# Optimization experiments

Measured on AMD Instinct MI355X. Metric: run time of the kernel, lower is better.

Reference implementation:

```python
import jax, jax.numpy as jnp
import numpy as np

DIM = 256
D_STATE = 32
EXPAND = 2
E = EXPAND * DIM            # d_inner = 512
DT_RANK = (DIM + 15) // 16  # 16 (mamba default ceil(d_model/16))
D_CONV = 4                  # mamba default causal conv width
B = 4
L = 1024


def layernorm(x, g, b, eps=1e-5):
    m = jnp.mean(x, axis=-1, keepdims=True)
    v = jnp.var(x, axis=-1, keepdims=True)
    return (x - m) / jnp.sqrt(v + eps) * g + b


def dwconv(x_bcl, w, b, pad):
    # x_bcl: [B,C,L], w: [C,1,K] depthwise
    y = jax.lax.conv_general_dilated(
        x_bcl, w, window_strides=(1,), padding=[pad],
        feature_group_count=x_bcl.shape[1],
        dimension_numbers=('NCW', 'OIW', 'NCW'))
    return y + b[None, :, None]


def selective_scan(u, dt, A, Bm, Cm, D):
    # u,dt: [B,L,E]; A: [E,N]; Bm,Cm: [B,L,N]; D: [E]
    dA = jnp.exp(dt[..., None] * A)                                # [B,L,E,N]
    dBu = dt[..., None] * Bm[:, :, None, :] * u[..., None]         # [B,L,E,N]

    def step(h, inp):
        dA_t, dBu_t = inp
        h = dA_t * h + dBu_t
        return h, h

    h0 = jnp.zeros((u.shape[0], E, D_STATE), u.dtype)
    _, hs = jax.lax.scan(step, h0, (dA.transpose(1, 0, 2, 3), dBu.transpose(1, 0, 2, 3)))
    y = jnp.einsum('lben,bln->ble', hs, Cm)                        # [B,L,E]
    return y + u * D


def mamba(x, in_proj_w, ssm_conv_w, ssm_conv_b, x_proj_w,
          dt_proj_w, dt_proj_b, A_log, Dp, out_proj_w):
    xz = x @ in_proj_w.T                     # [B,L,2E]
    xin, z = xz[..., :E], xz[..., E:]
    # causal depthwise conv (pad left D_CONV-1) + SiLU
    xc = dwconv(xin.transpose(0, 2, 1), ssm_conv_w, ssm_conv_b, (D_CONV - 1, 0))
    u = jax.nn.silu(xc).transpose(0, 2, 1)   # [B,L,E]
    dbl = u @ x_proj_w.T                      # [B,L,dt_rank+2N]
    dt_r = dbl[..., :DT_RANK]
    Bm = dbl[..., DT_RANK:DT_RANK + D_STATE]
    Cm = dbl[..., DT_RANK + D_STATE:]
    dt = jax.nn.softplus(dt_r @ dt_proj_w.T + dt_proj_b)  # [B,L,E]
    A = -jnp.exp(A_log)                                    # [E,N]
    y = selective_scan(u, dt, A, Bm, Cm, Dp)
    y = y * jax.nn.silu(z)
    return y @ out_proj_w.T


def setup_inputs() -> dict:
    key = jax.random.key(0)
    ks = jax.random.split(key, 12)
    f = lambda k, s, sc=0.02: jax.random.normal(k, s, jnp.float32) * sc
    dt_init = jnp.exp(jax.random.uniform(ks[10], (E,), jnp.float32,
                                         np.log(1e-3), np.log(1e-1)))
    dt_bias = dt_init + jnp.log(-jnp.expm1(-dt_init))  # inverse softplus
    A_log = jnp.log(jnp.tile(jnp.arange(1, D_STATE + 1, dtype=jnp.float32), (E, 1)))
    return {
        'x': jax.random.normal(ks[0], (B, L, DIM), jnp.float32),
        'norm1_g': jnp.ones((DIM,), jnp.float32), 'norm1_b': jnp.zeros((DIM,), jnp.float32),
        'conv_w': f(ks[1], (DIM, 1, 3), 0.1), 'conv_b': jnp.zeros((DIM,), jnp.float32),
        'in_proj_w': f(ks[2], (2 * E, DIM)),
        'ssm_conv_w': f(ks[3], (E, 1, D_CONV), 0.1), 'ssm_conv_b': jnp.zeros((E,), jnp.float32),
        'x_proj_w': f(ks[4], (DT_RANK + 2 * D_STATE, E)),
        'dt_proj_w': f(ks[5], (E, DT_RANK), 0.1), 'dt_proj_b': dt_bias,
        'A_log': A_log, 'Dp': jnp.ones((E,), jnp.float32),
        'out_proj_w': f(ks[6], (DIM, E)),
        'norm2_g': jnp.ones((DIM,), jnp.float32), 'norm2_b': jnp.zeros((DIM,), jnp.float32),
        'mlp_w1': f(ks[7], (4 * DIM, DIM)), 'mlp_b1': jnp.zeros((4 * DIM,), jnp.float32),
        'mlp_w2': f(ks[8], (DIM, 4 * DIM)), 'mlp_b2': jnp.zeros((DIM,), jnp.float32),
    }


def reference(x, norm1_g, norm1_b, conv_w, conv_b, in_proj_w, ssm_conv_w,
              ssm_conv_b, x_proj_w, dt_proj_w, dt_proj_b, A_log, Dp,
              out_proj_w, norm2_g, norm2_b, mlp_w1, mlp_b1, mlp_w2, mlp_b2):
    res = x
    h = layernorm(x, norm1_g, norm1_b)
    # local depthwise conv, kernel 3, same padding
    h_conv = dwconv(h.transpose(0, 2, 1), conv_w, conv_b, (1, 1)).transpose(0, 2, 1)
    h = mamba(h_conv + h, in_proj_w, ssm_conv_w, ssm_conv_b, x_proj_w,
              dt_proj_w, dt_proj_b, A_log, Dp, out_proj_w)
    h = res + h  # drop_path = identity (eval)
    m = layernorm(h, norm2_g, norm2_b)
    m = jax.nn.gelu(m @ mlp_w1.T + mlp_b1, approximate=False) @ mlp_w2.T + mlp_b2
    return h + m
```

## Files before the change

kernel.cpp:

```cpp
#include <hip/hip_runtime.h>
#include <hip/hip_bf16.h>
#include <math.h>

#define BATCH 4
#define LSEQ  1024
#define DIM   256
#define ESZ   512
#define NST   32
#define RNK   16
#define MROWS 4096
#define NCH   64
#define CHL   16

typedef __attribute__((ext_vector_type(8))) short bf16x8;
typedef __attribute__((ext_vector_type(4))) float f32x4;

__device__ __forceinline__ float silu_f(float v) { return v / (1.f + __expf(-v)); }
__device__ __forceinline__ float softplus_f(float v) {
    return (v > 20.f) ? v : log1pf(__expf(v));
}
__device__ __forceinline__ float bs2f(short s) {
    union { unsigned int u; float f; } v;
    v.u = ((unsigned int)(unsigned short)s) << 16;
    return v.f;
}
__device__ __forceinline__ short f2bs(float f) {
    __hip_bfloat16 h = __float2bfloat16(f);
    return *(short*)&h;
}

__global__ __launch_bounds__(256) void prep_kernel(
    const float* __restrict__ ipw, const float* __restrict__ opw,
    const float* __restrict__ w1,  const float* __restrict__ w2,
    const float* __restrict__ xpw, __hip_bfloat16* __restrict__ dst,
    const float* __restrict__ x, const float* __restrict__ g,
    const float* __restrict__ b, const float* __restrict__ cw,
    const float* __restrict__ cb, __hip_bfloat16* __restrict__ hm)
{
    if (blockIdx.x < 936) {
        int i = blockIdx.x * 256 + threadIdx.x;
        if (i >= 239616) return;
        const float* s; int off;
        if      (i < 65536)  { s = ipw; off = i; }
        else if (i < 98304)  { s = opw; off = i - 65536; }
        else if (i < 163840) { s = w1;  off = i - 98304; }
        else if (i < 229376) { s = w2;  off = i - 163840; }
        else                 { s = xpw; off = i - 229376; }
        float4 v = ((const float4*)s)[off];
        union { __hip_bfloat16 h[4]; short4 s4; } u;
        u.h[0] = __float2bfloat16(v.x);
        u.h[1] = __float2bfloat16(v.y);
        u.h[2] = __float2bfloat16(v.z);
        u.h[3] = __float2bfloat16(v.w);
        ((short4*)dst)[i] = u.s4;
        return;
    }
    const int row = blockIdx.x - 936;
    const int l   = row & (LSEQ - 1);
    const int d   = threadIdx.x;
    const float gc = g[d], bc = b[d];

    float xc = x[row * DIM + d];
    float xl = (l > 0)        ? x[(row - 1) * DIM + d] : 0.f;
    float xr = (l < LSEQ - 1) ? x[(row + 1) * DIM + d] : 0.f;

    float a[6] = { xc, xc * xc, xl, xl * xl, xr, xr * xr };
    #pragma unroll
    for (int o = 32; o > 0; o >>= 1)
        #pragma unroll
        for (int j = 0; j < 6; ++j) a[j] += __shfl_down(a[j], o, 64);
    __shared__ float red[4][6];
    if ((d & 63) == 0)
        #pragma unroll
        for (int j = 0; j < 6; ++j) red[d >> 6][j] = a[j];
    __syncthreads();
    float t[6];
    #pragma unroll
    for (int j = 0; j < 6; ++j)
        t[j] = red[0][j] + red[1][j] + red[2][j] + red[3][j];

    auto ln = [&](float v, float s, float s2) {
        float m  = s * (1.f / DIM);
        float vr = s2 * (1.f / DIM) - m * m;
        return (v - m) * rsqrtf(vr + 1e-5f) * gc + bc;
    };
    float ln_c = ln(xc, t[0], t[1]);
    float acc  = cw[d * 3 + 1] * ln_c + cb[d] + ln_c;
    if (l > 0)        acc += cw[d * 3 + 0] * ln(xl, t[2], t[3]);
    if (l < LSEQ - 1) acc += cw[d * 3 + 2] * ln(xr, t[4], t[5]);
    hm[row * DIM + d] = __float2bfloat16(acc);
}

#define EPI_NONE      0
#define EPI_GELU      2
#define EPI_RES       3
#define EPI_BIAS_RES  4

template <int BM, int BN, int EPI, int OUT_BF16>
__global__ __launch_bounds__(256) void gemm_lds(
    const __hip_bfloat16* __restrict__ A, int lda,
    const __hip_bfloat16* __restrict__ W, int ldw,
    void* __restrict__ Cout, int ldc, int K,
    const float* __restrict__ bias,
    const float* __restrict__ res, int ldres)
{
    constexpr int BK  = 64;
    constexpr int WTN = BN / 4;
    constexpr int BNF = WTN / 16;
    constexpr int AMF = BM / 16;
    constexpr int AIT = (BM * 8) / 256;
    constexpr int WIT = (BN * 8) / 256;

    __shared__ __hip_bfloat16 As[2][BM * BK];
    __shared__ __hip_bfloat16 Ws[2][BN * BK];

    const int tid  = threadIdx.x;
    const int lane = tid & 63;
    const int wave = tid >> 6;
    const int wn   = wave * WTN;
    const int m0   = blockIdx.x * BM;
    const int n0   = blockIdx.y * BN;
    const int q    = lane >> 4;
    const int lr   = lane & 15;
    const int sx   = (lr & 7) << 4;

    const __hip_bfloat16* Ab = A + (long)m0 * lda;
    const __hip_bfloat16* Wb = W + (long)n0 * ldw;

    f32x4 acc[AMF][BNF];
    #pragma unroll
    for (int i = 0; i < AMF; ++i)
        #pragma unroll
        for (int j = 0; j < BNF; ++j)
            acc[i][j] = (f32x4){0.f, 0.f, 0.f, 0.f};

    auto stage = [&](int s, int k0) {
        #pragma unroll
        for (int it = 0; it < AIT; ++it) {
            const int g   = it * 256 + tid;
            const int row = g >> 3;
            const int scc = (g & 7) ^ (row & 7);
            __builtin_amdgcn_global_load_lds(
                (const __attribute__((address_space(1))) void*)
                    (Ab + (long)row * lda + k0 + scc * 8),
                (__attribute__((address_space(3))) void*)
                    (&As[s][(it * 256 + wave * 64) * 8]),
                16, 0, 0);
        }
        #pragma unroll
        for (int it = 0; it < WIT; ++it) {
            const int g   = it * 256 + tid;
            const int row = g >> 3;
            const int scc = (g & 7) ^ (row & 7);
            __builtin_amdgcn_global_load_lds(
                (const __attribute__((address_space(1))) void*)
                    (Wb + (long)row * ldw + k0 + scc * 8),
                (__attribute__((address_space(3))) void*)
                    (&Ws[s][(it * 256 + wave * 64) * 8]),
                16, 0, 0);
        }
    };

    stage(0, 0);
    __syncthreads();

    int cur = 0;
    for (int k0 = 0; k0 < K; k0 += BK) {
        if (k0 + BK < K) stage(cur ^ 1, k0 + BK);
        #pragma unroll
        for (int ks = 0; ks < 2; ++ks) {
            const int co = (ks * 64 + q * 16) ^ sx;
            bf16x8 af[AMF], bfr[BNF];
            #pragma unroll
            for (int i = 0; i < AMF; ++i)
                af[i] = *(const bf16x8*)(
                    (const char*)&As[cur][0] + (i * 16 + lr) * 128 + co);
            #pragma unroll
            for (int j = 0; j < BNF; ++j)
                bfr[j] = *(const bf16x8*)(
                    (const char*)&Ws[cur][0] + (wn + j * 16 + lr) * 128 + co);
            #pragma unroll
            for (int i = 0; i < AMF; ++i)
                #pragma unroll
                for (int j = 0; j < BNF; ++j)
                    acc[i][j] = __builtin_amdgcn_mfma_f32_16x16x32_bf16(
                        af[i], bfr[j], acc[i][j], 0, 0, 0);
        }
        __syncthreads();
        cur ^= 1;
    }

    #pragma unroll
    for (int i = 0; i < AMF; ++i) {
        #pragma unroll
        for (int j = 0; j < BNF; ++j) {
            const int col  = n0 + wn + j * 16 + lr;
            const int rowb = m0 + i * 16 + q * 4;
            #pragma unroll
            for (int r = 0; r < 4; ++r) {
                const int row = rowb + r;
                float v = acc[i][j][r];
                if (EPI == EPI_GELU) {
                    v += bias[col];
                    v = 0.5f * v * (1.f + erff(v * 0.70710678118654752f));
                } else if (EPI == EPI_RES) {
                    v += res[(long)row * ldres + col];
                } else if (EPI == EPI_BIAS_RES) {
                    v += bias[col] + res[(long)row * ldres + col];
                }
                if (OUT_BF16)
                    ((__hip_bfloat16*)Cout)[(long)row * ldc + col] = __float2bfloat16(v);
                else
                    ((float*)Cout)[(long)row * ldc + col] = v;
            }
        }
    }
}

__global__ __launch_bounds__(256) void outproj_ln_kernel(
    const __hip_bfloat16* __restrict__ A,
    const __hip_bfloat16* __restrict__ W,
    const float* __restrict__ xres,
    const float* __restrict__ g, const float* __restrict__ b,
    float* __restrict__ hres,
    __hip_bfloat16* __restrict__ h1)
{
    constexpr int BM = 16, BN = 256, BK = 64, K = 512;
    __shared__ __hip_bfloat16 As[2][BM * BK];
    __shared__ __hip_bfloat16 Ws[2][BN * BK];
    __shared__ float lnt[BM][BN + 4];
    __shared__ float lnm[BM], lni[BM];

    const int tid  = threadIdx.x;
    const int lane = tid & 63;
    const int wave = tid >> 6;
    const int wn   = wave * 64;
    const int m0   = blockIdx.x * BM;
    const int q    = lane >> 4;
    const int lr   = lane & 15;
    const int sx   = (lr & 7) << 4;

    const __hip_bfloat16* Ab = A + (long)m0 * K;

    f32x4 acc[4];
    #pragma unroll
    for (int j = 0; j < 4; ++j) acc[j] = (f32x4){0.f, 0.f, 0.f, 0.f};

    auto stage = [&](int s, int k0) {
        if (wave < 2) {
            const int gA  = tid;
            const int row = gA >> 3;
            const int scc = (gA & 7) ^ (row & 7);
            __builtin_amdgcn_global_load_lds(
                (const __attribute__((address_space(1))) void*)
                    (Ab + (long)row * K + k0 + scc * 8),
                (__attribute__((address_space(3))) void*)
                    (&As[s][(wave * 64) * 8]),
                16, 0, 0);
        }
        #pragma unroll
        for (int it = 0; it < 8; ++it) {
            const int gW  = it * 256 + tid;
            const int row = gW >> 3;
            const int scc = (gW & 7) ^ (row & 7);
            __builtin_amdgcn_global_load_lds(
                (const __attribute__((address_space(1))) void*)
                    (W + (long)row * K + k0 + scc * 8),
                (__attribute__((address_space(3))) void*)
                    (&Ws[s][(it * 256 + wave * 64) * 8]),
                16, 0, 0);
        }
    };

    stage(0, 0);
    __syncthreads();

    int cur = 0;
    for (int k0 = 0; k0 < K; k0 += BK) {
        if (k0 + BK < K) stage(cur ^ 1, k0 + BK);
        #pragma unroll
        for (int ks = 0; ks < 2; ++ks) {
            const int co = (ks * 64 + q * 16) ^ sx;
            bf16x8 af = *(const bf16x8*)((const char*)&As[cur][0] + lr * 128 + co);
            #pragma unroll
            for (int j = 0; j < 4; ++j) {
                bf16x8 bfr = *(const bf16x8*)(
                    (const char*)&Ws[cur][0] + (wn + j * 16 + lr) * 128 + co);
                acc[j] = __builtin_amdgcn_mfma_f32_16x16x32_bf16(af, bfr, acc[j], 0, 0, 0);
            }
        }
        __syncthreads();
        cur ^= 1;
    }

    #pragma unroll
    for (int j = 0; j < 4; ++j) {
        const int col = wn + j * 16 + lr;
        #pragma unroll
        for (int r = 0; r < 4; ++r) {
            const int row = q * 4 + r;
            float v = acc[j][r] + xres[(long)(m0 + row) * DIM + col];
            hres[(long)(m0 + row) * DIM + col] = v;
            lnt[row][col] = v;
        }
    }
    __syncthreads();

    {
        const int rr = tid >> 4, cc = tid & 15;
        float s = 0.f, s2 = 0.f;
        #pragma unroll
        for (int k = 0; k < 16; ++k) {
            float v = lnt[rr][cc + k * 16];
            s += v; s2 += v * v;
        }
        #pragma unroll
        for (int m = 8; m > 0; m >>= 1) {
            s  += __shfl_xor(s,  m, 64);
            s2 += __shfl_xor(s2, m, 64);
        }
        if (cc == 0) {
            float mean = s * (1.f / DIM);
            float var  = s2 * (1.f / DIM) - mean * mean;
            lnm[rr] = mean;
            lni[rr] = rsqrtf(var + 1e-5f);
        }
    }
    __syncthreads();

    #pragma unroll
    for (int j = 0; j < 4; ++j) {
        const int col = wn + j * 16 + lr;
        const float gc = g[col], bc = b[col];
        #pragma unroll
        for (int r = 0; r < 4; ++r) {
            const int row = q * 4 + r;
            float v = lnt[row][col];
            h1[(long)(m0 + row) * DIM + col] =
                __float2bfloat16((v - lnm[row]) * lni[row] * gc + bc);
        }
    }
}

__global__ __launch_bounds__(256) void xproj_conv_mfma(
    const __hip_bfloat16* __restrict__ xz,
    const float* __restrict__ scw, const float* __restrict__ scb,
    const __hip_bfloat16* __restrict__ W,
    float* __restrict__ C)
{
    constexpr int LS = 72;
    __shared__ __hip_bfloat16 As[64 * LS];
    __shared__ __hip_bfloat16 Ws[80 * LS];
    const int tid  = threadIdx.x;
    const int lane = tid & 63;
    const int wave = tid >> 6;
    const int wm   = wave * 16;
    const int m0   = blockIdx.x * 64;
    const int srow = tid >> 3;
    const int scol = (tid & 7) * 8;
    const int q    = lane >> 4;
    const int lr   = lane & 15;

    f32x4 acc[5];
    #pragma unroll
    for (int j = 0; j < 5; ++j) acc[j] = (f32x4){0.f, 0.f, 0.f, 0.f};

    auto mk_u2 = [&](int k0, bf16x8& u0, bf16x8& u1) {
        const int e0 = k0 + scol;
        float4 w4[8]; float cbv[8];
        #pragma unroll
        for (int j = 0; j < 8; ++j) {
            w4[j]  = *(const float4*)(scw + (e0 + j) * 4);
            cbv[j] = scb[e0 + j];
        }
        #pragma unroll
        for (int r = 0; r < 2; ++r) {
            const int bl = m0 + r * 32 + srow;
            const int l  = bl & (LSEQ - 1);
            const __hip_bfloat16* xp = xz + (long)bl * 1024 + e0;
            bf16x8 x3 = *(const bf16x8*)(xp);
            bf16x8 x0 = (l >= 3) ? *(const bf16x8*)(xp - 3 * 1024) : (bf16x8){0,0,0,0,0,0,0,0};
            bf16x8 x1 = (l >= 2) ? *(const bf16x8*)(xp - 2 * 1024) : (bf16x8){0,0,0,0,0,0,0,0};
            bf16x8 x2 = (l >= 1) ? *(const bf16x8*)(xp - 1 * 1024) : (bf16x8){0,0,0,0,0,0,0,0};
            bf16x8 o;
            #pragma unroll
            for (int j = 0; j < 8; ++j) {
                float a = cbv[j]
                    + w4[j].x * bs2f(x0[j]) + w4[j].y * bs2f(x1[j])
                    + w4[j].z * bs2f(x2[j]) + w4[j].w * bs2f(x3[j]);
                o[j] = f2bs(silu_f(a));
            }
            if (r == 0) u0 = o; else u1 = o;
        }
    };

    bf16x8 uc[2];
    float4 wr[3];
    mk_u2(0, uc[0], uc[1]);
    #pragma unroll
    for (int r = 0; r < 3; ++r) {
        int row = r * 32 + srow;
        wr[r] = (row < 80) ? *(const float4*)(W + (long)row * 512 + scol)
                           : make_float4(0.f, 0.f, 0.f, 0.f);
    }

    for (int k0 = 0; k0 < 512; k0 += 64) {
        __syncthreads();
        #pragma unroll
        for (int r = 0; r < 2; ++r)
            *(bf16x8*)(&As[(r * 32 + srow) * LS + scol]) = uc[r];
        #pragma unroll
        for (int r = 0; r < 3; ++r) {
            int row = r * 32 + srow;
            if (row < 80) *(float4*)(&Ws[row * LS + scol]) = wr[r];
        }
        __syncthreads();
        if (k0 + 64 < 512) {
            mk_u2(k0 + 64, uc[0], uc[1]);
            #pragma unroll
            for (int r = 0; r < 3; ++r) {
                int row = r * 32 + srow;
                if (row < 80)
                    wr[r] = *(const float4*)(W + (long)row * 512 + k0 + 64 + scol);
            }
        }
        #pragma unroll
        for (int ks = 0; ks < 2; ++ks) {
            bf16x8 af = *(const bf16x8*)(&As[(wm + lr) * LS + ks * 32 + q * 8]);
            #pragma unroll
            for (int j = 0; j < 5; ++j) {
                bf16x8 bf = *(const bf16x8*)(&Ws[(j * 16 + lr) * LS + ks * 32 + q * 8]);
                acc[j] = __builtin_amdgcn_mfma_f32_16x16x32_bf16(af, bf, acc[j], 0, 0, 0);
            }
        }
    }
    #pragma unroll
    for (int j = 0; j < 5; ++j)
        #pragma unroll
        for (int r = 0; r < 4; ++r)
            C[(long)(m0 + wm + q * 4 + r) * 80 + j * 16 + lr] = acc[j][r];
}

__global__ __launch_bounds__(256) void scan_s1(
    const __hip_bfloat16* __restrict__ xz, const float* __restrict__ dbl,
    const float* __restrict__ dtw, const float* __restrict__ dtb,
    const float* __restrict__ A_log,
    const float* __restrict__ scw, const float* __restrict__ scb,
    __hip_bfloat16* __restrict__ P, __hip_bfloat16* __restrict__ Q)
{
    const int tid = threadIdx.x;
    const int e  = ((blockIdx.x & 1) << 8) + tid;
    const int bc = blockIdx.x >> 1;
    const int c  = bc & (NCH - 1);
    const int b  = bc >> 6;

    __shared__ float sD[CHL][80];
    for (int g = tid; g < CHL * 20; g += 256) {
        int r = g / 20, cg = (g % 20) * 4;
        *(float4*)&sD[r][cg] =
            *(const float4*)(dbl + ((long)b * LSEQ + c * CHL + r) * 80 + cg);
    }

    float Aen[NST];
    #pragma unroll
    for (int qd = 0; qd < 8; ++qd) {
        float4 a4 = *(const float4*)(A_log + e * NST + qd * 4);
        Aen[qd * 4 + 0] = -__expf(a4.x);
        Aen[qd * 4 + 1] = -__expf(a4.y);
        Aen[qd * 4 + 2] = -__expf(a4.z);
        Aen[qd * 4 + 3] = -__expf(a4.w);
    }
    float cw4[4];
    #pragma unroll
    for (int k = 0; k < 4; ++k) cw4[k] = scw[e * 4 + k];
    const float cbe = scb[e];

    float4 wq[4];
    #pragma unroll
    for (int qd = 0; qd < 4; ++qd)
        wq[qd] = *(const float4*)(dtw + e * RNK + qd * 4);
    const float dtbe = dtb[e];

    const int l0 = c * CHL;
    const long rowbase = ((long)b * LSEQ) * 1024 + e;
    float xw0, xw1, xw2;
    if (c == 0) { xw0 = xw1 = xw2 = 0.f; }
    else {
        xw0 = __bfloat162float(xz[rowbase + (long)(l0 - 3) * 1024]);
        xw1 = __bfloat162float(xz[rowbase + (long)(l0 - 2) * 1024]);
        xw2 = __bfloat162float(xz[rowbase + (long)(l0 - 1) * 1024]);
    }

    float Pv[NST], Qv[NST];
    #pragma unroll
    for (int n = 0; n < NST; ++n) { Pv[n] = 1.f; Qv[n] = 0.f; }
    __syncthreads();

    for (int t = 0; t < CHL; ++t) {
        const int l = l0 + t;
        float xw3 = __bfloat162float(xz[rowbase + (long)l * 1024]);
        float u = silu_f(cbe + cw4[0]*xw0 + cw4[1]*xw1 + cw4[2]*xw2 + cw4[3]*xw3);
        xw0 = xw1; xw1 = xw2; xw2 = xw3;

        float4 d0 = *(const float4*)&sD[t][0];
        float4 d1 = *(const float4*)&sD[t][4];
        float4 d2 = *(const float4*)&sD[t][8];
        float4 d3 = *(const float4*)&sD[t][12];
        float raw = dtbe
            + wq[0].x*d0.x + wq[0].y*d0.y + wq[0].z*d0.z + wq[0].w*d0.w
            + wq[1].x*d1.x + wq[1].y*d1.y + wq[1].z*d1.z + wq[1].w*d1.w
            + wq[2].x*d2.x + wq[2].y*d2.y + wq[2].z*d2.z + wq[2].w*d2.w
            + wq[3].x*d3.x + wq[3].y*d3.y + wq[3].z*d3.z + wq[3].w*d3.w;
        float dt = softplus_f(raw);
        float xx = dt * u;

        #pragma unroll
        for (int qd = 0; qd < 8; ++qd) {
            float4 b4 = *(const float4*)&sD[t][16 + qd * 4];
            #pragma unroll
            for (int j = 0; j < 4; ++j) {
                const int n = qd * 4 + j;
                float bn = (j == 0) ? b4.x : (j == 1) ? b4.y : (j == 2) ? b4.z : b4.w;
                float dA = __expf(dt * Aen[n]);
                Pv[n] *= dA;
                Qv[n] = fmaf(dA, Qv[n], xx * bn);
            }
        }
    }
    const long pb = ((long)(b * NCH + c) * NST) * ESZ + e;
    #pragma unroll
    for (int n = 0; n < NST; ++n) {
        P[pb + (long)n * ESZ] = __float2bfloat16(Pv[n]);
        Q[pb + (long)n * ESZ] = __float2bfloat16(Qv[n]);
    }
}

__global__ __launch_bounds__(256) void scan_s2(
    __hip_bfloat16* __restrict__ P, const __hip_bfloat16* __restrict__ Q)
{
    const int tg = blockIdx.x * 256 + threadIdx.x;
    const int e  = tg & (ESZ - 1);
    const int n  = (tg >> 9) & (NST - 1);
    const int b  = tg >> 14;
    float h = 0.f;
    #pragma unroll 16
    for (int c = 0; c < NCH; ++c) {
        const long idx = ((long)(b * NCH + c) * NST + n) * ESZ + e;
        float Pv = __bfloat162float(P[idx]);
        float Qv = __bfloat162float(Q[idx]);
        P[idx] = __float2bfloat16(h);
        h = fmaf(Pv, h, Qv);
    }
}

__global__ __launch_bounds__(256) void scan_s3(
    const __hip_bfloat16* __restrict__ xz, const float* __restrict__ dbl,
    const float* __restrict__ dtw, const float* __restrict__ dtb,
    const float* __restrict__ A_log,
    const float* __restrict__ scw, const float* __restrict__ scb,
    const float* __restrict__ Dp, const __hip_bfloat16* __restrict__ H,
    __hip_bfloat16* __restrict__ yg)
{
    const int tid = threadIdx.x;
    const int e  = ((blockIdx.x & 1) << 8) + tid;
    const int bc = blockIdx.x >> 1;
    const int c  = bc & (NCH - 1);
    const int b  = bc >> 6;

    __shared__ float sD[CHL][80];
    for (int g = tid; g < CHL * 20; g += 256) {
        int r = g / 20, cg = (g % 20) * 4;
        *(float4*)&sD[r][cg] =
            *(const float4*)(dbl + ((long)b * LSEQ + c * CHL + r) * 80 + cg);
    }

    float Aen[NST];
    #pragma unroll
    for (int qd = 0; qd < 8; ++qd) {
        float4 a4 = *(const float4*)(A_log + e * NST + qd * 4);
        Aen[qd * 4 + 0] = -__expf(a4.x);
        Aen[qd * 4 + 1] = -__expf(a4.y);
        Aen[qd * 4 + 2] = -__expf(a4.z);
        Aen[qd * 4 + 3] = -__expf(a4.w);
    }
    float cw4[4];
    #pragma unroll
    for (int k = 0; k < 4; ++k) cw4[k] = scw[e * 4 + k];
    const float cbe = scb[e];
    const float dpe = Dp[e];

    float4 wq[4];
    #pragma unroll
    for (int qd = 0; qd < 4; ++qd)
        wq[qd] = *(const float4*)(dtw + e * RNK + qd * 4);
    const float dtbe = dtb[e];

    float h[NST];
    const long pb = ((long)(b * NCH + c) * NST) * ESZ + e;
    #pragma unroll
    for (int n = 0; n < NST; ++n)
        h[n] = __bfloat162float(H[pb + (long)n * ESZ]);

    const int l0 = c * CHL;
    const long rowbase = ((long)b * LSEQ) * 1024 + e;
    float xw0, xw1, xw2;
    if (c == 0) { xw0 = xw1 = xw2 = 0.f; }
    else {
        xw0 = __bfloat162float(xz[rowbase + (long)(l0 - 3) * 1024]);
        xw1 = __bfloat162float(xz[rowbase + (long)(l0 - 2) * 1024]);
        xw2 = __bfloat162float(xz[rowbase + (long)(l0 - 1) * 1024]);
    }
    __syncthreads();

    for (int t = 0; t < CHL; ++t) {
        const int l = l0 + t;
        const long bl = (long)b * LSEQ + l;
        float xw3 = __bfloat162float(xz[rowbase + (long)l * 1024]);
        float u = silu_f(cbe + cw4[0]*xw0 + cw4[1]*xw1 + cw4[2]*xw2 + cw4[3]*xw3);
        xw0 = xw1; xw1 = xw2; xw2 = xw3;

        float4 d0 = *(const float4*)&sD[t][0];
        float4 d1 = *(const float4*)&sD[t][4];
        float4 d2 = *(const float4*)&sD[t][8];
        float4 d3 = *(const float4*)&sD[t][12];
        float raw = dtbe
            + wq[0].x*d0.x + wq[0].y*d0.y + wq[0].z*d0.z + wq[0].w*d0.w
            + wq[1].x*d1.x + wq[1].y*d1.y + wq[1].z*d1.z + wq[1].w*d1.w
            + wq[2].x*d2.x + wq[2].y*d2.y + wq[2].z*d2.z + wq[2].w*d2.w
            + wq[3].x*d3.x + wq[3].y*d3.y + wq[3].z*d3.z + wq[3].w*d3.w;
        float dt = softplus_f(raw);
        float xx = dt * u;

        float y = 0.f;
        #pragma unroll
        for (int qd = 0; qd < 8; ++qd) {
            float4 b4 = *(const float4*)&sD[t][16 + qd * 4];
            float4 c4 = *(const float4*)&sD[t][48 + qd * 4];
            #pragma unroll
            for (int j = 0; j < 4; ++j) {
                const int n = qd * 4 + j;
                float bn = (j == 0) ? b4.x : (j == 1) ? b4.y : (j == 2) ? b4.z : b4.w;
                float cn = (j == 0) ? c4.x : (j == 1) ? c4.y : (j == 2) ? c4.z : c4.w;
                float dA = __expf(dt * Aen[n]);
                h[n] = fmaf(dA, h[n], xx * bn);
                y = fmaf(h[n], cn, y);
            }
        }
        y += u * dpe;
        float z = __bfloat162float(xz[rowbase + (long)l * 1024 + ESZ]);
        yg[bl * ESZ + e] = __float2bfloat16(y * silu_f(z));
    }
}

extern "C" void kernel_launch(void* const* d_in, const int* in_sizes, int n_in,
                              void* d_out, int out_size, void* d_ws, size_t ws_size,
                              hipStream_t stream)
{
    const float* x    = (const float*)d_in[0];
    const float* n1g  = (const float*)d_in[1];
    const float* n1b  = (const float*)d_in[2];
    const float* cw   = (const float*)d_in[3];
    const float* cb   = (const float*)d_in[4];
    const float* ipw  = (const float*)d_in[5];
    const float* scw  = (const float*)d_in[6];
    const float* scb  = (const float*)d_in[7];
    const float* xpw  = (const float*)d_in[8];
    const float* dtw  = (const float*)d_in[9];
    const float* dtbi = (const float*)d_in[10];
    const float* alog = (const float*)d_in[11];
    const float* dp   = (const float*)d_in[12];
    const float* opw  = (const float*)d_in[13];
    const float* n2g  = (const float*)d_in[14];
    const float* n2b  = (const float*)d_in[15];
    const float* w1   = (const float*)d_in[16];
    const float* b1   = (const float*)d_in[17];
    const float* w2   = (const float*)d_in[18];
    const float* b2   = (const float*)d_in[19];
    float* out = (float*)d_out;

    float* ws = (float*)d_ws;
    __hip_bfloat16* hmb  = (__hip_bfloat16*)(ws + 0);
    __hip_bfloat16* xzb  = (__hip_bfloat16*)(ws + 524288);
    float*          dbl  = ws + 3670016;
    __hip_bfloat16* P    = (__hip_bfloat16*)(ws + 5046272);
    __hip_bfloat16* Q    = (__hip_bfloat16*)(ws + 7143424);
    __hip_bfloat16* ygb  = (__hip_bfloat16*)(ws + 9240576);
    float*          hres = ws + 10289152;
    __hip_bfloat16* h1b  = (__hip_bfloat16*)(ws + 11337728);
    __hip_bfloat16* midb = (__hip_bfloat16*)(ws + 11862016);
    __hip_bfloat16* wb   = (__hip_bfloat16*)(ws + 13959168);
    __hip_bfloat16* ipwb = wb;
    __hip_bfloat16* opwb = wb + 262144;
    __hip_bfloat16* w1b  = wb + 393216;
    __hip_bfloat16* w2b  = wb + 655360;
    __hip_bfloat16* xpwb = wb + 917504;

    prep_kernel<<<5032, 256, 0, stream>>>(ipw, opw, w1, w2, xpw, wb,
                                          x, n1g, n1b, cw, cb, hmb);
    gemm_lds<64, 128, EPI_NONE, 1><<<dim3(64, 8), 256, 0, stream>>>(
        hmb, 256, ipwb, 256, xzb, 1024, 256, nullptr, nullptr, 0);
    xproj_conv_mfma<<<64, 256, 0, stream>>>(xzb, scw, scb, xpwb, dbl);
    scan_s1<<<512, 256, 0, stream>>>(xzb, dbl, dtw, dtbi, alog, scw, scb, P, Q);
    scan_s2<<<256, 256, 0, stream>>>(P, Q);
    scan_s3<<<512, 256, 0, stream>>>(xzb, dbl, dtw, dtbi, alog, scw, scb, dp, P, ygb);
    outproj_ln_kernel<<<256, 256, 0, stream>>>(ygb, opwb, x, n2g, n2b, hres, h1b);
    gemm_lds<64, 128, EPI_GELU, 1><<<dim3(64, 8), 256, 0, stream>>>(
        h1b, 256, w1b, 256, midb, 1024, 256, b1, nullptr, 0);
    gemm_lds<64, 64, EPI_BIAS_RES, 0><<<dim3(64, 4), 256, 0, stream>>>(
        midb, 1024, w2b, 1024, out, 256, 1024, b2, hres, 256);
}
```

Baseline: 234.3 us.

## Prefetch two stages ahead with vmcnt waits instead of full syncthreads in GEMMs

Restructures the double-buffered LDS pipeline in the generic GEMM and the out-proj+LayerNorm kernel. Two K-tiles are issued up front, and each iteration waits with s_waitcnt vmcnt for only the older tile's loads. The next load is issued after a barrier once its buffer is free, so global loads overlap a full compute step instead of being drained by __syncthreads. It also spreads the out-proj A-tile load across all four waves (32 lanes each) so the per-wave vmcnt counts are uniform. The hand-coded vmcnt counts depend on an exact per-wave load count, so a mismatch could cause races.

Measured after the change: 231.7 us. No clear change (-1.1%).

```diff
diff --git a/kernel.cpp b/kernel.cpp
--- a/kernel.cpp
+++ b/kernel.cpp
@@ -27,6 +27,18 @@
 __device__ __forceinline__ short f2bs(float f) {
     __hip_bfloat16 h = __float2bfloat16(f);
     return *(short*)&h;
+}
+
+template <int N> __device__ __forceinline__ void waitvm() {
+    if constexpr (N == 0) asm volatile("s_waitcnt vmcnt(0)" ::: "memory");
+    else if constexpr (N == 4) asm volatile("s_waitcnt vmcnt(4)" ::: "memory");
+    else if constexpr (N == 6) asm volatile("s_waitcnt vmcnt(6)" ::: "memory");
+    else if constexpr (N == 9) asm volatile("s_waitcnt vmcnt(9)" ::: "memory");
+    else static_assert(N == 0, "add literal");
+}
+__device__ __forceinline__ void fence_sched() {
+    __builtin_amdgcn_sched_barrier(0);
+    asm volatile("" ::: "memory");
 }
 
 __global__ __launch_bounds__(256) void prep_kernel(
@@ -110,6 +122,7 @@
     constexpr int AMF = BM / 16;
     constexpr int AIT = (BM * 8) / 256;
     constexpr int WIT = (BN * 8) / 256;
+    constexpr int NLD = AIT + WIT;
 
     __shared__ __hip_bfloat16 As[2][BM * BK];
     __shared__ __hip_bfloat16 Ws[2][BN * BK];
@@ -162,11 +175,13 @@
     };
 
     stage(0, 0);
-    __syncthreads();
+    if (BK < K) stage(1, BK);
 
     int cur = 0;
     for (int k0 = 0; k0 < K; k0 += BK) {
-        if (k0 + BK < K) stage(cur ^ 1, k0 + BK);
+        if (k0 + BK < K) waitvm<NLD>(); else waitvm<0>();
+        __builtin_amdgcn_s_barrier();
+        fence_sched();
         #pragma unroll
         for (int ks = 0; ks < 2; ++ks) {
             const int co = (ks * 64 + q * 16) ^ sx;
@@ -186,7 +201,10 @@
                     acc[i][j] = __builtin_amdgcn_mfma_f32_16x16x32_bf16(
                         af[i], bfr[j], acc[i][j], 0, 0, 0);
         }
-        __syncthreads();
+        fence_sched();
+        __builtin_amdgcn_s_barrier();
+        fence_sched();
+        if (k0 + 2 * BK < K) stage(cur, k0 + 2 * BK);
         cur ^= 1;
     }
 
@@ -226,6 +244,7 @@
     __hip_bfloat16* __restrict__ h1)
 {
     constexpr int BM = 16, BN = 256, BK = 64, K = 512;
+    constexpr int NLD = 9;
     __shared__ __hip_bfloat16 As[2][BM * BK];
     __shared__ __hip_bfloat16 Ws[2][BN * BK];
     __shared__ float lnt[BM][BN + 4];
@@ -247,16 +266,18 @@
     for (int j = 0; j < 4; ++j) acc[j] = (f32x4){0.f, 0.f, 0.f, 0.f};
 
     auto stage = [&](int s, int k0) {
-        if (wave < 2) {
-            const int gA  = tid;
-            const int row = gA >> 3;
-            const int scc = (gA & 7) ^ (row & 7);
-            __builtin_amdgcn_global_load_lds(
-                (const __attribute__((address_space(1))) void*)
-                    (Ab + (long)row * K + k0 + scc * 8),
-                (__attribute__((address_space(3))) void*)
-                    (&As[s][(wave * 64) * 8]),
-                16, 0, 0);
+        {
+            const int ch = wave * 32 + lane;
+            if (lane < 32) {
+                const int row = ch >> 3;
+                const int scc = (ch & 7) ^ (row & 7);
+                __builtin_amdgcn_global_load_lds(
+                    (const __attribute__((address_space(1))) void*)
+                        (Ab + (long)row * K + k0 + scc * 8),
+                    (__attribute__((address_space(3))) void*)
+                        (&As[s][(wave * 32) * 8]),
+                    16, 0, 0);
+            }
         }
         #pragma unroll
         for (int it = 0; it < 8; ++it) {
@@ -273,11 +294,13 @@
     };
 
     stage(0, 0);
-    __syncthreads();
+    stage(1, BK);
 
     int cur = 0;
     for (int k0 = 0; k0 < K; k0 += BK) {
-        if (k0 + BK < K) stage(cur ^ 1, k0 + BK);
+        if (k0 + BK < K) waitvm<NLD>(); else waitvm<0>();
+        __builtin_amdgcn_s_barrier();
+        fence_sched();
         #pragma unroll
         for (int ks = 0; ks < 2; ++ks) {
             const int co = (ks * 64 + q * 16) ^ sx;
@@ -289,7 +312,10 @@
                 acc[j] = __builtin_amdgcn_mfma_f32_16x16x32_bf16(af, bfr, acc[j], 0, 0, 0);
             }
         }
-        __syncthreads();
+        fence_sched();
+        __builtin_amdgcn_s_barrier();
+        fence_sched();
+        if (k0 + 2 * BK < K) stage(cur, k0 + 2 * BK);
         cur ^= 1;
     }
 
```
